# Kernel optimization log

Measured on AMD Instinct MI355X. Metric: run time of the kernel, lower is better.

The kernel has to match this reference:

```python
import jax, jax.numpy as jnp
import numpy as np

IN_F = 4096
OUT_F = 11008
GROUP_SIZE = 128
NUM_GROUPS = (IN_F + GROUP_SIZE - 1) // GROUP_SIZE  # 32
N_HIGH = int(OUT_F * 0.25)   # 2752
N_LOW = OUT_F - N_HIGH       # 8256
B, S = 2, 2048


def setup_inputs() -> dict:
    key = jax.random.key(0)
    ks = jax.random.split(key, 9)
    x = jax.random.normal(ks[0], (B, S, IN_F), dtype=jnp.float32)
    # INT8 symmetric codes for high-precision columns
    high_prec_weight = jax.random.randint(ks[1], (IN_F, N_HIGH), -128, 128, dtype=jnp.int32)
    # per-group, per-column scales (positive, realistic magnitude)
    high_prec_scales = jax.random.uniform(ks[2], (NUM_GROUPS, N_HIGH), jnp.float32, 1e-4, 2e-2)
    # 4-bit asymmetric codes in [0, 15]
    low_prec_weight = jax.random.randint(ks[3], (IN_F, N_LOW), 0, 16, dtype=jnp.int32)
    low_prec_scales = jax.random.uniform(ks[4], (IN_F, 1), jnp.float32, 1e-4, 2e-2)
    low_prec_scales2 = jax.random.uniform(ks[5], (1, N_LOW), jnp.float32, 0.5, 2.0)
    low_prec_zeros = jnp.round(jax.random.uniform(ks[6], (IN_F, 1), jnp.float32, 0.0, 15.0))
    # inverse column permutation restoring original order
    col_indices_inv = jax.random.permutation(ks[7], OUT_F).astype(jnp.int64)
    bias = jax.random.normal(ks[8], (OUT_F,), dtype=jnp.float32) * 0.02
    return {
        "x": x,
        "high_prec_weight": high_prec_weight,
        "high_prec_scales": high_prec_scales,
        "low_prec_weight": low_prec_weight,
        "low_prec_scales": low_prec_scales,
        "low_prec_scales2": low_prec_scales2,
        "low_prec_zeros": low_prec_zeros,
        "col_indices_inv": col_indices_inv,
        "bias": bias,
    }


def _dequantize(high_w, high_scales, low_w, low_s1, low_s2, low_z, col_inv):
    # High: group-wise symmetric INT8 dequant. K divisible by GROUP_SIZE here (no pad).
    w_high = (high_w.astype(jnp.float32)
              .reshape(NUM_GROUPS, GROUP_SIZE, N_HIGH)
              * high_scales[:, None, :]).reshape(IN_F, N_HIGH)
    # Low: SINQ dual-scale asymmetric dequant: ((q - z) * s1) * s2
    w_low = (low_w.astype(jnp.float32) - low_z) * low_s1 * low_s2
    # Reassemble original column order: W_kn [in_features, out_features]
    w = jnp.concatenate([w_high, w_low], axis=1)[:, col_inv]
    return w


def reference(x, high_prec_weight, high_prec_scales, low_prec_weight,
              low_prec_scales, low_prec_scales2, low_prec_zeros,
              col_indices_inv, bias):
    w_kn = _dequantize(high_prec_weight, high_prec_scales, low_prec_weight,
                       low_prec_scales, low_prec_scales2, low_prec_zeros,
                       col_indices_inv)
    # F.linear(x, W_original) with W_original = w_kn.T  ->  x @ w_kn
    out = jnp.einsum('bsk,kn->bsn', x, w_kn) + bias
    return out
```

## Files before the change

kernel.cpp:

```cpp
#include <hip/hip_runtime.h>
#include <hip/hip_bf16.h>

#define IN_F   4096
#define OUT_F  11008
#define NHIGH  2752
#define NLOW   8256
#define M_TOT  4096

typedef __attribute__((ext_vector_type(8))) short bf16x8;
typedef __attribute__((ext_vector_type(4))) float f32x4;

__device__ __forceinline__ short f2bf(float f) {
    union { float f; unsigned u; } v; v.f = f;
    unsigned r = (v.u + 0x7fffu + ((v.u >> 16) & 1u)) >> 16;
    return (short)(r & 0xffffu);
}

__device__ __forceinline__ void async16(const void* g, const void* l) {
    __builtin_amdgcn_global_load_lds(
        (const __attribute__((address_space(1))) unsigned int*)g,
        (__attribute__((address_space(3))) unsigned int*)l, 16, 0, 0);
}

__global__ void fwd_perm_kernel(const int* __restrict__ cinv, int* __restrict__ fwd) {
    int n = blockIdx.x * blockDim.x + threadIdx.x;
    if (n < OUT_F) fwd[cinv[n]] = n;
}

__global__ void cvt_x_kernel(const float* __restrict__ x, short* __restrict__ xb) {
    const int nv = (M_TOT * IN_F) / 8;
    for (int i = blockIdx.x * blockDim.x + threadIdx.x; i < nv;
         i += gridDim.x * blockDim.x) {
        const float4* p = (const float4*)(x + (long)i * 8);
        float4 a = p[0], b = p[1];
        bf16x8 o;
        o[0] = f2bf(a.x); o[1] = f2bf(a.y); o[2] = f2bf(a.z); o[3] = f2bf(a.w);
        o[4] = f2bf(b.x); o[5] = f2bf(b.y); o[6] = f2bf(b.z); o[7] = f2bf(b.w);
        *(bf16x8*)(xb + (long)i * 8) = o;
    }
}

__global__ void dequant_kernel(const int* __restrict__ hw, const float* __restrict__ hs,
                               const int* __restrict__ lw, const float* __restrict__ s1,
                               const float* __restrict__ s2, const float* __restrict__ zp,
                               const int* __restrict__ fwd,
                               short* __restrict__ wt) {
    __shared__ short tile[64 * 66];
    const int t  = threadIdx.x;
    const int c0 = blockIdx.x * 64;
    const int k0 = blockIdx.y * 64;
    const int cl = t & 63;
    const int w  = t >> 6;

    if (c0 < NHIGH) {
        const int ci = c0 + cl;
        #pragma unroll
        for (int i = 0; i < 16; ++i) {
            const int kl = w + 4 * i;
            const int k  = k0 + kl;
            float val = (float)hw[(long)k * NHIGH + ci] * hs[(k >> 7) * NHIGH + ci];
            tile[cl * 66 + kl] = f2bf(val);
        }
    } else {
        const int ci = c0 - NHIGH + cl;
        const float s2v = s2[ci];
        #pragma unroll
        for (int i = 0; i < 16; ++i) {
            const int kl = w + 4 * i;
            const int k  = k0 + kl;
            float val = ((float)lw[(long)k * NLOW + ci] - zp[k]) * s1[k] * s2v;
            tile[cl * 66 + kl] = f2bf(val);
        }
    }
    __syncthreads();
    const int oc = t >> 2;
    const int kq = (t & 3) * 16;
    bf16x8 o0, o1;
    #pragma unroll
    for (int j = 0; j < 8; ++j) {
        o0[j] = tile[oc * 66 + kq + j];
        o1[j] = tile[oc * 66 + kq + 8 + j];
    }
    const int ndst = fwd[c0 + oc];
    short* dst = wt + (long)ndst * IN_F + k0 + kq;
    *(bf16x8*)dst       = o0;
    *(bf16x8*)(dst + 8) = o1;
}

#define BM 128
#define BN 128
#define BK 64
#define KT (IN_F / BK)
#define NTILES (OUT_F / BN)
#define MTILES (M_TOT / BM)
#define NWG (NTILES * MTILES)
#define GSUP 8

__global__ __launch_bounds__(256, 2) void gemm_kernel(
    const short* __restrict__ A,
    const short* __restrict__ Bt,
    const float* __restrict__ bias,
    float* __restrict__ C) {
    __shared__ __align__(16) short As[BM * BK];
    __shared__ __align__(16) short Bs[BN * BK];

    const int t    = threadIdx.x;
    const int lane = t & 63;
    const int w    = t >> 6;
    const int wr   = w >> 1, wc = w & 1;

    const int swz   = (blockIdx.x % 8) * (NWG / 8) + blockIdx.x / 8;
    const int sr    = swz / (GSUP * NTILES);
    const int in_sr = swz % (GSUP * NTILES);
    const int nb    = in_sr / GSUP;
    const int mb    = sr * GSUP + (in_sr % GSUP);
    const int m0    = mb * BM;
    const int n0    = nb * BN;

    const int srow = (w * 4) * 8 + (lane >> 3);
    const int scol = (lane & 7) * 8;
    const short* gA = A  + (long)(m0 + srow) * IN_F + scol;
    const short* gB = Bt + (long)(n0 + srow) * IN_F + scol;

    f32x4 acc[4][4];
    #pragma unroll
    for (int mi = 0; mi < 4; ++mi)
        #pragma unroll
        for (int ni = 0; ni < 4; ++ni)
            acc[mi][ni] = (f32x4){0.f, 0.f, 0.f, 0.f};

    for (int kt = 0; kt < KT; ++kt) {
        const int kofs = kt * BK;
        #pragma unroll
        for (int j = 0; j < 4; ++j) {
            async16(gA + kofs + j * 8 * IN_F, (char*)As + (w * 4 + j) * 1024);
            async16(gB + kofs + j * 8 * IN_F, (char*)Bs + (w * 4 + j) * 1024);
        }
        __syncthreads();
        #pragma unroll
        for (int kk = 0; kk < 2; ++kk) {
            bf16x8 af[4], bfr[4];
            #pragma unroll
            for (int mi = 0; mi < 4; ++mi)
                af[mi] = *(const bf16x8*)(As + (wr * 64 + mi * 16 + (lane & 15)) * BK
                                             + kk * 32 + (lane >> 4) * 8);
            #pragma unroll
            for (int ni = 0; ni < 4; ++ni)
                bfr[ni] = *(const bf16x8*)(Bs + (wc * 64 + ni * 16 + (lane & 15)) * BK
                                              + kk * 32 + (lane >> 4) * 8);
            #pragma unroll
            for (int mi = 0; mi < 4; ++mi)
                #pragma unroll
                for (int ni = 0; ni < 4; ++ni)
                    acc[mi][ni] = __builtin_amdgcn_mfma_f32_16x16x32_bf16(
                        af[mi], bfr[ni], acc[mi][ni], 0, 0, 0);
        }
        __syncthreads();
    }

    const int crow  = m0 + wr * 64 + (lane >> 4) * 4;
    const int ccol0 = n0 + wc * 64 + (lane & 15);
    #pragma unroll
    for (int ni = 0; ni < 4; ++ni) {
        const float bv = bias[ccol0 + ni * 16];
        #pragma unroll
        for (int mi = 0; mi < 4; ++mi) {
            #pragma unroll
            for (int r = 0; r < 4; ++r) {
                C[(long)(crow + mi * 16 + r) * OUT_F + ccol0 + ni * 16] =
                    acc[mi][ni][r] + bv;
            }
        }
    }
}

extern "C" void kernel_launch(void* const* d_in, const int* in_sizes, int n_in,
                              void* d_out, int out_size, void* d_ws, size_t ws_size,
                              hipStream_t stream) {
    const float* x    = (const float*)d_in[0];
    const int*   hw   = (const int*)d_in[1];
    const float* hs   = (const float*)d_in[2];
    const int*   lw   = (const int*)d_in[3];
    const float* s1   = (const float*)d_in[4];
    const float* s2   = (const float*)d_in[5];
    const float* zp   = (const float*)d_in[6];
    const int*   cinv = (const int*)d_in[7];
    const float* bias = (const float*)d_in[8];
    float*       out  = (float*)d_out;

    short* wt  = (short*)d_ws;
    short* xb  = (short*)((char*)d_ws + (size_t)OUT_F * IN_F * 2);
    int*   fwd = (int*)((char*)d_ws + (size_t)OUT_F * IN_F * 2
                                    + (size_t)M_TOT * IN_F * 2);

    fwd_perm_kernel<<<(OUT_F + 255) / 256, 256, 0, stream>>>(cinv, fwd);
    cvt_x_kernel<<<2048, 256, 0, stream>>>(x, xb);
    dequant_kernel<<<dim3(OUT_F / 64, IN_F / 64), 256, 0, stream>>>(
        hw, hs, lw, s1, s2, zp, fwd, wt);
    gemm_kernel<<<NWG, 256, 0, stream>>>(xb, wt, bias, out);
}
```

Measured before the change: 482.2 us.

## Rewrite GEMM as 256x256 8-wave double-buffered LDS pipeline with swizzle

The GEMM moves from 128x128 tiles with 4 waves to 256x256 tiles with 8 waves, giving each wave a 128x64 output. It uses double-buffered LDS (128KB) with XOR-swizzled layout and fine-grained async global-to-LDS loads interleaved between MFMA quadrants. Explicit waitcnt/barrier control and setprio are meant to overlap memory traffic with matrix math and avoid LDS bank conflicts. The cost is larger LDS and register use, roughly one block per CU, and a more fragile hand-written schedule.

After: 412.0 us. 14.6% less time.

```diff
diff --git a/kernel.cpp b/kernel.cpp
--- a/kernel.cpp
+++ b/kernel.cpp
@@ -87,87 +87,166 @@
     *(bf16x8*)(dst + 8) = o1;
 }
 
-#define BM 128
-#define BN 128
+#define BM 256
+#define BN 256
 #define BK 64
 #define KT (IN_F / BK)
-#define NTILES (OUT_F / BN)
-#define MTILES (M_TOT / BM)
-#define NWG (NTILES * MTILES)
-#define GSUP 8
-
-__global__ __launch_bounds__(256, 2) void gemm_kernel(
+#define NTIL (OUT_F / BN)
+#define MTIL (M_TOT / BM)
+#define NWG2 (NTIL * MTIL)
+
+#define BAR()    __builtin_amdgcn_s_barrier()
+#define LGKM0()  asm volatile("s_waitcnt lgkmcnt(0)" ::: "memory")
+#define VMC(N)   asm volatile("s_waitcnt vmcnt(" #N ")" ::: "memory")
+
+__global__ __launch_bounds__(512, 2) void gemm_kernel(
     const short* __restrict__ A,
     const short* __restrict__ Bt,
     const float* __restrict__ bias,
     float* __restrict__ C) {
-    __shared__ __align__(16) short As[BM * BK];
-    __shared__ __align__(16) short Bs[BN * BK];
+    __shared__ __align__(16) short lds_s[65536];
+    char* const lds = (char*)lds_s;
 
     const int t    = threadIdx.x;
     const int lane = t & 63;
     const int w    = t >> 6;
-    const int wr   = w >> 1, wc = w & 1;
-
-    const int swz   = (blockIdx.x % 8) * (NWG / 8) + blockIdx.x / 8;
-    const int sr    = swz / (GSUP * NTILES);
-    const int in_sr = swz % (GSUP * NTILES);
-    const int nb    = in_sr / GSUP;
-    const int mb    = sr * GSUP + (in_sr % GSUP);
+    const int wr   = w >> 2;
+    const int wc   = w & 3;
+
+    const int swz   = (blockIdx.x % 8) * (NWG2 / 8) + blockIdx.x / 8;
+    const int sr    = swz / (4 * NTIL);
+    const int in_sr = swz % (4 * NTIL);
+    const int nb    = in_sr / 4;
+    const int mb    = sr * 4 + (in_sr & 3);
     const int m0    = mb * BM;
     const int n0    = nb * BN;
 
-    const int srow = (w * 4) * 8 + (lane >> 3);
-    const int scol = (lane & 7) * 8;
-    const short* gA = A  + (long)(m0 + srow) * IN_F + scol;
-    const short* gB = Bt + (long)(n0 + srow) * IN_F + scol;
-
-    f32x4 acc[4][4];
+    const int srow = w * 8 + (lane >> 3);
+    const int scb  = ((lane & 7) ^ (lane >> 3)) * 16;
+    const char* gA0 = (const char*)A  + (long)(m0 + srow) * (IN_F * 2) + scb;
+    const char* gB0 = (const char*)Bt + (long)(n0 + srow) * (IN_F * 2) + scb;
+
+    const int rl  = (lane & 15) * 128;
+    const int kb0 = ((lane >> 4) * 16) ^ ((lane & 7) << 4);
+    const int kb1 = kb0 ^ 64;
+
+#define STAGE(gbase, region_off, h, ktile) do {                                  \
+        const char* _g = (gbase) + (long)((h) * 128) * (IN_F * 2) + (ktile) * 128; \
+        char* _l = lds + (region_off) + (h) * 16384 + w * 1024;                  \
+        async16(_g,                      _l);                                    \
+        async16(_g + (long)64 * (IN_F * 2), _l + 8192);                          \
+    } while (0)
+
+    f32x4 acc[8][4];
     #pragma unroll
-    for (int mi = 0; mi < 4; ++mi)
-        #pragma unroll
-        for (int ni = 0; ni < 4; ++ni)
-            acc[mi][ni] = (f32x4){0.f, 0.f, 0.f, 0.f};
-
-    for (int kt = 0; kt < KT; ++kt) {
-        const int kofs = kt * BK;
-        #pragma unroll
-        for (int j = 0; j < 4; ++j) {
-            async16(gA + kofs + j * 8 * IN_F, (char*)As + (w * 4 + j) * 1024);
-            async16(gB + kofs + j * 8 * IN_F, (char*)Bs + (w * 4 + j) * 1024);
-        }
-        __syncthreads();
-        #pragma unroll
-        for (int kk = 0; kk < 2; ++kk) {
-            bf16x8 af[4], bfr[4];
-            #pragma unroll
-            for (int mi = 0; mi < 4; ++mi)
-                af[mi] = *(const bf16x8*)(As + (wr * 64 + mi * 16 + (lane & 15)) * BK
-                                             + kk * 32 + (lane >> 4) * 8);
-            #pragma unroll
-            for (int ni = 0; ni < 4; ++ni)
-                bfr[ni] = *(const bf16x8*)(Bs + (wc * 64 + ni * 16 + (lane & 15)) * BK
-                                              + kk * 32 + (lane >> 4) * 8);
-            #pragma unroll
-            for (int mi = 0; mi < 4; ++mi)
-                #pragma unroll
-                for (int ni = 0; ni < 4; ++ni)
-                    acc[mi][ni] = __builtin_amdgcn_mfma_f32_16x16x32_bf16(
-                        af[mi], bfr[ni], acc[mi][ni], 0, 0, 0);
-        }
-        __syncthreads();
-    }
-
-    const int crow  = m0 + wr * 64 + (lane >> 4) * 4;
-    const int ccol0 = n0 + wc * 64 + (lane & 15);
+    for (int i = 0; i < 8; ++i)
+        #pragma unroll
+        for (int j = 0; j < 4; ++j)
+            acc[i][j] = (f32x4){0.f, 0.f, 0.f, 0.f};
+
+    bf16x8 a[4][2], b0[2][2], b1[2][2];
+
+#define RD_A(buf, mq) do {                                                       \
+        char* _p = lds + (buf) * 65536 + wr * 16384 + (mq) * 8192 + rl;          \
+        _Pragma("unroll")                                                        \
+        for (int _j = 0; _j < 4; ++_j) {                                         \
+            a[_j][0] = *(const bf16x8*)(_p + _j * 2048 + kb0);                   \
+            a[_j][1] = *(const bf16x8*)(_p + _j * 2048 + kb1);                   \
+        }                                                                        \
+    } while (0)
+
+#define RD_B(buf, nq, breg) do {                                                 \
+        char* _p = lds + (buf) * 65536 + 32768 + wc * 8192 + (nq) * 4096 + rl;   \
+        _Pragma("unroll")                                                        \
+        for (int _n = 0; _n < 2; ++_n) {                                         \
+            breg[_n][0] = *(const bf16x8*)(_p + _n * 2048 + kb0);                \
+            breg[_n][1] = *(const bf16x8*)(_p + _n * 2048 + kb1);                \
+        }                                                                        \
+    } while (0)
+
+#define MMA_Q(mq, nq, breg) do {                                                 \
+        __builtin_amdgcn_s_setprio(1);                                           \
+        _Pragma("unroll")                                                        \
+        for (int _j = 0; _j < 4; ++_j)                                           \
+        _Pragma("unroll")                                                        \
+        for (int _n = 0; _n < 2; ++_n) {                                         \
+            acc[(mq)*4+_j][(nq)*2+_n] = __builtin_amdgcn_mfma_f32_16x16x32_bf16( \
+                a[_j][0], breg[_n][0], acc[(mq)*4+_j][(nq)*2+_n], 0, 0, 0);      \
+            acc[(mq)*4+_j][(nq)*2+_n] = __builtin_amdgcn_mfma_f32_16x16x32_bf16( \
+                a[_j][1], breg[_n][1], acc[(mq)*4+_j][(nq)*2+_n], 0, 0, 0);      \
+        }                                                                        \
+        __builtin_amdgcn_s_setprio(0);                                           \
+    } while (0)
+
+    STAGE(gA0, 0,     0, 0);
+    STAGE(gA0, 0,     1, 0);
+    STAGE(gB0, 32768, 0, 0);
+    STAGE(gB0, 32768, 1, 0);
+    STAGE(gA0, 65536, 0, 1);
+    VMC(2);
+    BAR();
+
+    #pragma unroll 1
+    for (int it = 0; it < KT / 2; ++it) {
+        const int kt1 = 2 * it + 1;
+        const int kt2 = (2 * it + 2 < KT) ? 2 * it + 2 : KT - 1;
+        const int kt3 = (2 * it + 3 < KT) ? 2 * it + 3 : KT - 1;
+
+        RD_A(0, 0); RD_B(0, 0, b0);
+        STAGE(gA0, 65536 + 0,     1, kt1);
+        BAR(); LGKM0();
+        MMA_Q(0, 0, b0);
+        BAR();
+        RD_B(0, 1, b1);
+        STAGE(gB0, 65536 + 32768, 0, kt1);
+        BAR(); LGKM0();
+        MMA_Q(0, 1, b1);
+        BAR();
+        RD_A(0, 1);
+        STAGE(gB0, 65536 + 32768, 1, kt1);
+        BAR(); LGKM0();
+        MMA_Q(1, 1, b1);
+        BAR();
+        STAGE(gA0, 0,             0, kt2);
+        BAR();
+        MMA_Q(1, 0, b0);
+        VMC(2);
+        BAR();
+
+        RD_A(1, 0); RD_B(1, 0, b0);
+        STAGE(gA0, 0,             1, kt2);
+        BAR(); LGKM0();
+        MMA_Q(0, 0, b0);
+        BAR();
+        RD_B(1, 1, b1);
+        STAGE(gB0, 32768,         0, kt2);
+        BAR(); LGKM0();
+        MMA_Q(0, 1, b1);
+        BAR();
+        RD_A(1, 1);
+        STAGE(gB0, 32768,         1, kt2);
+        BAR(); LGKM0();
+        MMA_Q(1, 1, b1);
+        BAR();
+        STAGE(gA0, 65536,         0, kt3);
+        BAR();
+        MMA_Q(1, 0, b0);
+        VMC(2);
+        BAR();
+    }
+
+    asm volatile("s_waitcnt vmcnt(0)" ::: "memory");
+
+    const int er = m0 + wr * 128 + (lane >> 4) * 4;
+    const int ec = n0 + wc * 64 + (lane & 15);
     #pragma unroll
     for (int ni = 0; ni < 4; ++ni) {
-        const float bv = bias[ccol0 + ni * 16];
-        #pragma unroll
-        for (int mi = 0; mi < 4; ++mi) {
+        const float bv = bias[ec + ni * 16];
+        #pragma unroll
+        for (int mi = 0; mi < 8; ++mi) {
             #pragma unroll
             for (int r = 0; r < 4; ++r) {
-                C[(long)(crow + mi * 16 + r) * OUT_F + ccol0 + ni * 16] =
+                C[(long)(er + mi * 16 + r) * OUT_F + ec + ni * 16] =
                     acc[mi][ni][r] + bv;
             }
         }
@@ -197,5 +276,5 @@
     cvt_x_kernel<<<2048, 256, 0, stream>>>(x, xb);
     dequant_kernel<<<dim3(OUT_F / 64, IN_F / 64), 256, 0, stream>>>(
         hw, hs, lw, s1, s2, zp, fwd, wt);
-    gemm_kernel<<<NWG, 256, 0, stream>>>(xb, wt, bias, out);
-}
+    gemm_kernel<<<NWG2, 512, 0, stream>>>(xb, wt, bias, out);
+}
```
